# Kernel tuning notes

Measured on AMD Instinct MI355X. Metric: run time of the kernel, lower is better.

## Reference

```python
import jax, jax.numpy as jnp
import numpy as np

BN_EPS = 1e-5
NORM_EPS = 1e-12  # F.normalize eps


def setup_inputs() -> dict:
    key = jax.random.key(0)
    ks = jax.random.split(key, 4)
    B, C1, H, W = 32, 2048, 32, 32
    D1, D2, NC = 1024, 256, 1000
    x = jax.random.normal(ks[0], (B, C1, H, W), dtype=jnp.float32)
    w1 = jax.random.normal(ks[1], (D1, C1), dtype=jnp.float32) * 0.01  # init_weights normal 0.01
    gamma = jnp.ones((D1,), dtype=jnp.float32)
    beta = jnp.zeros((D1,), dtype=jnp.float32)
    w2 = jax.random.normal(ks[2], (D2, D1), dtype=jnp.float32) * 0.01
    prototypes = jax.random.normal(ks[3], (NC, D2), dtype=jnp.float32)
    return {"x": x, "w1": w1, "gamma": gamma, "beta": beta, "w2": w2, "prototypes": prototypes}


def _l2_normalize(v, axis):
    n = jnp.sqrt(jnp.sum(v * v, axis=axis, keepdims=True))
    return v / jnp.maximum(n, NORM_EPS)


def reference(x, w1, gamma, beta, w2, prototypes):
    # 1x1 conv (no bias) == channel matmul
    h = jnp.einsum('bchw,dc->bdhw', x, w1)  # [B,D1,H,W]
    # BatchNorm2d (training-mode batch stats, affine)
    mean = jnp.mean(h, axis=(0, 2, 3), keepdims=True)
    var = jnp.var(h, axis=(0, 2, 3), keepdims=True)
    h = (h - mean) * jax.lax.rsqrt(var + BN_EPS)
    h = h * gamma[None, :, None, None] + beta[None, :, None, None]
    h = jax.nn.relu(h)
    # final 1x1 conv
    f = jnp.einsum('bchw,dc->bdhw', h, w2)  # [B,D2,H,W]
    B, D, H, W = f.shape
    f = f.reshape(B, D, H * W)  # flatten(2)
    # L2-normalize over channel dim per spatial position, and prototypes per row
    f_norm = _l2_normalize(f, axis=1)           # [B,D,HW]
    p_norm = _l2_normalize(prototypes, axis=1)  # [N,D]
    # einsum('bdc,nd->bnc').sum(-1) == contract d then sum c in one fused einsum
    sim = jnp.einsum('bdc,nd->bn', f_norm, p_norm)  # [B,N]
    return sim
```

## Files before the change

kernel.cpp:

```cpp
#include <hip/hip_runtime.h>

typedef __bf16 bf16;
typedef __bf16 bf16x4 __attribute__((ext_vector_type(4)));
typedef __bf16 bf16x8 __attribute__((ext_vector_type(8)));
typedef float  f32x4  __attribute__((ext_vector_type(4)));

__device__ inline void async_copy16(void* lds, const void* g) {
  __builtin_amdgcn_global_load_lds((const __attribute__((address_space(1))) void*)g,
                                   (__attribute__((address_space(3))) void*)lds,
                                   16, 0, 0);
}

__global__ __launch_bounds__(256)
void f2bf_kernel(const float* __restrict__ in, bf16* __restrict__ out, int n4) {
  int i = blockIdx.x * 256 + threadIdx.x;
  if (i < n4) {
    float4 v = ((const float4*)in)[i];
    bf16x4 o;
    o[0] = (bf16)v.x; o[1] = (bf16)v.y; o[2] = (bf16)v.z; o[3] = (bf16)v.w;
    ((bf16x4*)out)[i] = o;
  }
}

__global__ __launch_bounds__(256)
void transpose_convert(const float* __restrict__ x, bf16* __restrict__ xb) {
  __shared__ float tile[64][65];
  const int tx = threadIdx.x & 15;
  const int ty = threadIdx.x >> 4;
  const int b   = blockIdx.z;
  const int c0  = blockIdx.y * 64;
  const int hw0 = blockIdx.x * 64;
  const float* xp = x + ((size_t)b * 2048 + c0) * 1024 + hw0;
#pragma unroll
  for (int i = 0; i < 4; ++i) {
    const int c = i * 16 + ty;
    const float4 v = *(const float4*)(xp + (size_t)c * 1024 + tx * 4);
    tile[c][tx * 4 + 0] = v.x; tile[c][tx * 4 + 1] = v.y;
    tile[c][tx * 4 + 2] = v.z; tile[c][tx * 4 + 3] = v.w;
  }
  __syncthreads();
  bf16* op = xb + ((size_t)b * 1024 + hw0) * 2048 + c0;
#pragma unroll
  for (int i = 0; i < 4; ++i) {
    const int hw = i * 16 + ty;
    bf16x4 o;
    o[0] = (bf16)tile[tx * 4 + 0][hw];
    o[1] = (bf16)tile[tx * 4 + 1][hw];
    o[2] = (bf16)tile[tx * 4 + 2][hw];
    o[3] = (bf16)tile[tx * 4 + 3][hw];
    *(bf16x4*)(op + (size_t)hw * 2048 + tx * 4) = o;
  }
}

__global__ __launch_bounds__(256, 4)
void gemm1(const bf16* __restrict__ A, const bf16* __restrict__ Bt,
           bf16* __restrict__ Cb, float* __restrict__ S1, float* __restrict__ S2) {
  __shared__ __align__(16) bf16 As[128 * 64];
  __shared__ __align__(16) bf16 Bs[128 * 64];
  const int K = 2048, N = 1024;
  const int tid  = threadIdx.x;
  const int wave = tid >> 6;
  const int lane = tid & 63;
  const int id = blockIdx.x;
  const int bm = (id & 7) * 32 + ((id >> 3) >> 3);
  const int bn = (id >> 3) & 7;
  const int wr = wave >> 1, wc = wave & 1;
  const int srow = lane >> 3;
  const int scol = (lane & 7) ^ srow;

  f32x4 acc[4][4];
#pragma unroll
  for (int r = 0; r < 4; ++r)
#pragma unroll
    for (int c = 0; c < 4; ++c) acc[r][c] = (f32x4){0.f, 0.f, 0.f, 0.f};

  const bf16* Ag = A + (size_t)(bm * 128) * K;
  const bf16* Bg = Bt + (size_t)(bn * 128) * K;

  const int mrow = lane & 15;
  const int kq = lane >> 4;
  const int sw = mrow & 7;
  const bf16* Asw = As + (wr * 64) * 64;
  const bf16* Bsw = Bs + (wc * 64) * 64;

  for (int k0 = 0; k0 < K; k0 += 64) {
#pragma unroll
    for (int j = 0; j < 4; ++j) {
      const int row = j * 32 + wave * 8;
      async_copy16((void*)(As + row * 64),
                   (const void*)(Ag + (size_t)(row + srow) * K + k0 + scol * 8));
      async_copy16((void*)(Bs + row * 64),
                   (const void*)(Bg + (size_t)(row + srow) * K + k0 + scol * 8));
    }
    __syncthreads();
#pragma unroll
    for (int kk = 0; kk < 2; ++kk) {
      bf16x8 af[4], bfr[4];
      const int lc = kk * 4 + kq;
#pragma unroll
      for (int r = 0; r < 4; ++r)
        af[r] = *(const bf16x8*)(Asw + (r * 16 + mrow) * 64 + ((lc ^ sw) * 8));
#pragma unroll
      for (int c = 0; c < 4; ++c)
        bfr[c] = *(const bf16x8*)(Bsw + (c * 16 + mrow) * 64 + ((lc ^ sw) * 8));
#pragma unroll
      for (int r = 0; r < 4; ++r)
#pragma unroll
        for (int c = 0; c < 4; ++c)
          acc[r][c] = __builtin_amdgcn_mfma_f32_16x16x32_bf16(af[r], bfr[c], acc[r][c], 0, 0, 0);
    }
    __syncthreads();
  }

  const int crow = (lane >> 4) * 4;
  const int ccol = lane & 15;
#pragma unroll
  for (int r = 0; r < 4; ++r)
#pragma unroll
    for (int c = 0; c < 4; ++c)
#pragma unroll
      for (int i = 0; i < 4; ++i) {
        const int gm = bm * 128 + wr * 64 + r * 16 + crow + i;
        const int gn = bn * 128 + wc * 64 + c * 16 + ccol;
        Cb[(size_t)gm * N + gn] = (bf16)acc[r][c][i];
      }

  float s1[4], s2[4];
#pragma unroll
  for (int c = 0; c < 4; ++c) {
    float a = 0.f, b = 0.f;
#pragma unroll
    for (int r = 0; r < 4; ++r)
#pragma unroll
      for (int i = 0; i < 4; ++i) { const float v = acc[r][c][i]; a += v; b += v * v; }
#pragma unroll
    for (int msk = 16; msk < 64; msk <<= 1) { a += __shfl_xor(a, msk, 64); b += __shfl_xor(b, msk, 64); }
    s1[c] = a; s2[c] = b;
  }
  float* S1s = (float*)As;
  float* S2s = S1s + 256;
  if ((lane & 15) == lane) {
#pragma unroll
    for (int c = 0; c < 4; ++c) {
      S1s[wr * 128 + wc * 64 + c * 16 + lane] = s1[c];
      S2s[wr * 128 + wc * 64 + c * 16 + lane] = s2[c];
    }
  }
  __syncthreads();
  if (tid < 128) {
    atomicAdd(&S1[bn * 128 + tid], S1s[tid] + S1s[128 + tid]);
    atomicAdd(&S2[bn * 128 + tid], S2s[tid] + S2s[128 + tid]);
  }
}

__global__ __launch_bounds__(256)
void bn_finalize(const float* __restrict__ S1, const float* __restrict__ S2,
                 const float* __restrict__ gamma, const float* __restrict__ beta,
                 float* __restrict__ scale, float* __restrict__ shift) {
  const int d = blockIdx.x * 256 + threadIdx.x;
  const float inv_n = 1.0f / 32768.0f;
  const float mean = S1[d] * inv_n;
  const float var  = S2[d] * inv_n - mean * mean;
  const float rstd = rsqrtf(var + 1e-5f);
  const float sc = gamma[d] * rstd;
  scale[d] = sc;
  shift[d] = beta[d] - mean * sc;
}

__global__ __launch_bounds__(512, 4)
void gemm2f(const bf16* __restrict__ A, const bf16* __restrict__ Bt,
            const float* __restrict__ scale, const float* __restrict__ shift,
            float* __restrict__ g) {
  __shared__ __align__(16) bf16 As[128 * 64];
  __shared__ __align__(16) bf16 Bs[256 * 64];
  const int K = 1024;
  const int tid  = threadIdx.x;
  const int wave = tid >> 6;
  const int lane = tid & 63;
  const int bm = blockIdx.x;
  const int wr = wave >> 2, wc = wave & 3;
  const int srow = lane >> 3;
  const int scol = (lane & 7) ^ srow;

  f32x4 acc[4][4];
#pragma unroll
  for (int r = 0; r < 4; ++r)
#pragma unroll
    for (int c = 0; c < 4; ++c) acc[r][c] = (f32x4){0.f, 0.f, 0.f, 0.f};

  const bf16* Ag = A + (size_t)(bm * 128) * K;

  const int mrow = lane & 15;
  const int kq = lane >> 4;
  const int sw = mrow & 7;
  const bf16* Asw = As + (wr * 64) * 64;
  const bf16* Bsw = Bs + (wc * 64) * 64;

  for (int k0 = 0; k0 < K; k0 += 64) {
#pragma unroll
    for (int j = 0; j < 2; ++j) {
      const int row = wave * 16 + j * 8;
      async_copy16((void*)(As + row * 64),
                   (const void*)(Ag + (size_t)(row + srow) * K + k0 + scol * 8));
    }
#pragma unroll
    for (int j = 0; j < 4; ++j) {
      const int row = wave * 32 + j * 8;
      async_copy16((void*)(Bs + row * 64),
                   (const void*)(Bt + (size_t)(row + srow) * K + k0 + scol * 8));
    }
    __syncthreads();
#pragma unroll
    for (int kk = 0; kk < 2; ++kk) {
      const int lc = kk * 4 + kq;
      const int kbase = k0 + lc * 8;
      const float4 sc0 = *(const float4*)(scale + kbase);
      const float4 sc1 = *(const float4*)(scale + kbase + 4);
      const float4 sh0 = *(const float4*)(shift + kbase);
      const float4 sh1 = *(const float4*)(shift + kbase + 4);
      const float scv[8] = {sc0.x, sc0.y, sc0.z, sc0.w, sc1.x, sc1.y, sc1.z, sc1.w};
      const float shv[8] = {sh0.x, sh0.y, sh0.z, sh0.w, sh1.x, sh1.y, sh1.z, sh1.w};
      bf16x8 af[4], bfr[4];
#pragma unroll
      for (int r = 0; r < 4; ++r) {
        bf16x8 a = *(const bf16x8*)(Asw + (r * 16 + mrow) * 64 + ((lc ^ sw) * 8));
#pragma unroll
        for (int j = 0; j < 8; ++j)
          a[j] = (bf16)fmaxf(0.f, fmaf((float)a[j], scv[j], shv[j]));
        af[r] = a;
      }
#pragma unroll
      for (int c = 0; c < 4; ++c)
        bfr[c] = *(const bf16x8*)(Bsw + (c * 16 + mrow) * 64 + ((lc ^ sw) * 8));
#pragma unroll
      for (int r = 0; r < 4; ++r)
#pragma unroll
        for (int c = 0; c < 4; ++c)
          acc[r][c] = __builtin_amdgcn_mfma_f32_16x16x32_bf16(af[r], bfr[c], acc[r][c], 0, 0, 0);
    }
    __syncthreads();
  }

  float* ss4   = (float*)As;
  float* inv_s = ss4 + 512;
  const int q = lane >> 4;
#pragma unroll
  for (int r = 0; r < 4; ++r) {
    float ssv[4];
#pragma unroll
    for (int i = 0; i < 4; ++i) {
      float s = 0.f;
#pragma unroll
      for (int c = 0; c < 4; ++c) { const float v = acc[r][c][i]; s += v * v; }
#pragma unroll
      for (int msk = 1; msk < 16; msk <<= 1) s += __shfl_xor(s, msk, 64);
      ssv[i] = s;
    }
    if ((lane & 15) == 0)
#pragma unroll
      for (int i = 0; i < 4; ++i)
        ss4[wc * 128 + wr * 64 + r * 16 + q * 4 + i] = ssv[i];
  }
  __syncthreads();
  if (tid < 128) {
    const float rs = ss4[tid] + ss4[128 + tid] + ss4[256 + tid] + ss4[384 + tid];
    inv_s[tid] = 1.0f / fmaxf(sqrtf(rs), 1e-12f);
  }
  __syncthreads();
  const int b = bm >> 3;
  const int ccol = lane & 15;
#pragma unroll
  for (int c = 0; c < 4; ++c) {
    float gl = 0.f;
#pragma unroll
    for (int r = 0; r < 4; ++r)
#pragma unroll
      for (int i = 0; i < 4; ++i)
        gl += acc[r][c][i] * inv_s[wr * 64 + r * 16 + q * 4 + i];
#pragma unroll
    for (int msk = 16; msk < 64; msk <<= 1) gl += __shfl_xor(gl, msk, 64);
    if ((lane & 48) == 0)
      atomicAdd(&g[b * 256 + wc * 64 + c * 16 + ccol], gl);
  }
}

__global__ __launch_bounds__(256)
void sim_kernel(const float* __restrict__ g, const float* __restrict__ protos,
                float* __restrict__ out) {
  const int wave = threadIdx.x >> 6, lane = threadIdx.x & 63;
  const int n = blockIdx.x * 4 + wave;
  const float4 p = *(const float4*)(protos + (size_t)n * 256 + lane * 4);
  float ss = p.x * p.x + p.y * p.y + p.z * p.z + p.w * p.w;
#pragma unroll
  for (int msk = 1; msk < 64; msk <<= 1) ss += __shfl_xor(ss, msk, 64);
  const float inv = 1.0f / fmaxf(sqrtf(ss), 1e-12f);
  const float px = p.x * inv, py = p.y * inv, pz = p.z * inv, pw = p.w * inv;
  for (int b = 0; b < 32; ++b) {
    const float4 gv = *(const float4*)(g + b * 256 + lane * 4);
    float d = px * gv.x + py * gv.y + pz * gv.z + pw * gv.w;
#pragma unroll
    for (int msk = 1; msk < 64; msk <<= 1) d += __shfl_xor(d, msk, 64);
    if (lane == 0) out[b * 1000 + n] = d;
  }
}

extern "C" void kernel_launch(void* const* d_in, const int* in_sizes, int n_in,
                              void* d_out, int out_size, void* d_ws, size_t ws_size,
                              hipStream_t stream) {
  const float* x      = (const float*)d_in[0];
  const float* w1     = (const float*)d_in[1];
  const float* gamma  = (const float*)d_in[2];
  const float* beta   = (const float*)d_in[3];
  const float* w2     = (const float*)d_in[4];
  const float* protos = (const float*)d_in[5];
  float* out = (float*)d_out;

  char* ws = (char*)d_ws;
  bf16*  xb    = (bf16*)(ws);
  bf16*  hb    = (bf16*)(ws + (size_t)134217728);
  bf16*  w1b   = (bf16*)(ws + (size_t)201326592);
  bf16*  w2b   = (bf16*)(ws + (size_t)205520896);
  float* S1    = (float*)(ws + (size_t)206045184);
  float* S2    = (float*)(ws + (size_t)206049280);
  float* g     = (float*)(ws + (size_t)206053376);
  float* scale = (float*)(ws + (size_t)206086144);
  float* shift = (float*)(ws + (size_t)206090240);

  hipMemsetAsync(S1, 0, 40960, stream);

  f2bf_kernel<<<2048, 256, 0, stream>>>(w1, w1b, 524288);
  f2bf_kernel<<<256, 256, 0, stream>>>(w2, w2b, 65536);
  transpose_convert<<<dim3(16, 32, 32), 256, 0, stream>>>(x, xb);
  gemm1<<<2048, 256, 0, stream>>>(xb, w1b, hb, S1, S2);
  bn_finalize<<<4, 256, 0, stream>>>(S1, S2, gamma, beta, scale, shift);
  gemm2f<<<256, 512, 0, stream>>>(hb, w2b, scale, shift, g);
  sim_kernel<<<250, 256, 0, stream>>>(g, protos, out);
}
```

Baseline: 612.2 us.

## Fuse x transpose and bf16 conversion into gemm1 A-tile loading

Drops the separate transpose_convert pass and has gemm1 read fp32 x directly, transposing 4x4 sub-blocks with cross-lane shuffles and writing swizzled bf16 into LDS. This removes a 256MB read plus 128MB write/read round trip of the bf16 copy of x. In exchange, gemm1 reads fp32 A (twice the bytes per tile) synchronously instead of via async LDS loads, its occupancy bound drops to 3, and the main loop carries extra shuffle work. gemm2f also stages the BN scale and shift arrays in LDS instead of reading them from global memory every k step.

```diff
diff --git a/kernel.cpp b/kernel.cpp
--- a/kernel.cpp
+++ b/kernel.cpp
@@ -9,6 +9,19 @@
   __builtin_amdgcn_global_load_lds((const __attribute__((address_space(1))) void*)g,
                                    (__attribute__((address_space(3))) void*)lds,
                                    16, 0, 0);
+}
+
+__device__ inline void xpose4(float v[4], int cg) {
+  float a = (cg & 2) ? v[0] : v[2];
+  float b = (cg & 2) ? v[1] : v[3];
+  float ra = __shfl_xor(a, 32, 64);
+  float rb = __shfl_xor(b, 32, 64);
+  if (cg & 2) { v[0] = ra; v[1] = rb; } else { v[2] = ra; v[3] = rb; }
+  float c = (cg & 1) ? v[0] : v[1];
+  float d = (cg & 1) ? v[2] : v[3];
+  float rc = __shfl_xor(c, 16, 64);
+  float rd = __shfl_xor(d, 16, 64);
+  if (cg & 1) { v[0] = rc; v[2] = rd; } else { v[1] = rc; v[3] = rd; }
 }
 
 __global__ __launch_bounds__(256)
@@ -22,38 +35,8 @@
   }
 }
 
-__global__ __launch_bounds__(256)
-void transpose_convert(const float* __restrict__ x, bf16* __restrict__ xb) {
-  __shared__ float tile[64][65];
-  const int tx = threadIdx.x & 15;
-  const int ty = threadIdx.x >> 4;
-  const int b   = blockIdx.z;
-  const int c0  = blockIdx.y * 64;
-  const int hw0 = blockIdx.x * 64;
-  const float* xp = x + ((size_t)b * 2048 + c0) * 1024 + hw0;
-#pragma unroll
-  for (int i = 0; i < 4; ++i) {
-    const int c = i * 16 + ty;
-    const float4 v = *(const float4*)(xp + (size_t)c * 1024 + tx * 4);
-    tile[c][tx * 4 + 0] = v.x; tile[c][tx * 4 + 1] = v.y;
-    tile[c][tx * 4 + 2] = v.z; tile[c][tx * 4 + 3] = v.w;
-  }
-  __syncthreads();
-  bf16* op = xb + ((size_t)b * 1024 + hw0) * 2048 + c0;
-#pragma unroll
-  for (int i = 0; i < 4; ++i) {
-    const int hw = i * 16 + ty;
-    bf16x4 o;
-    o[0] = (bf16)tile[tx * 4 + 0][hw];
-    o[1] = (bf16)tile[tx * 4 + 1][hw];
-    o[2] = (bf16)tile[tx * 4 + 2][hw];
-    o[3] = (bf16)tile[tx * 4 + 3][hw];
-    *(bf16x4*)(op + (size_t)hw * 2048 + tx * 4) = o;
-  }
-}
-
-__global__ __launch_bounds__(256, 4)
-void gemm1(const bf16* __restrict__ A, const bf16* __restrict__ Bt,
+__global__ __launch_bounds__(256, 3)
+void gemm1(const float* __restrict__ X, const bf16* __restrict__ Bt,
            bf16* __restrict__ Cb, float* __restrict__ S1, float* __restrict__ S2) {
   __shared__ __align__(16) bf16 As[128 * 64];
   __shared__ __align__(16) bf16 Bs[128 * 64];
@@ -68,13 +51,22 @@
   const int srow = lane >> 3;
   const int scol = (lane & 7) ^ srow;
 
+  const int cg  = lane >> 4;
+  const int hw4 = lane & 15;
+  const int cgq = wave >> 1;
+  const int mh  = wave & 1;
+  const int ml  = mh * 64 + hw4 * 4 + cg;
+  const int mlsw = 2 * (ml & 7);
+
   f32x4 acc[4][4];
 #pragma unroll
   for (int r = 0; r < 4; ++r)
 #pragma unroll
     for (int c = 0; c < 4; ++c) acc[r][c] = (f32x4){0.f, 0.f, 0.f, 0.f};
 
-  const bf16* Ag = A + (size_t)(bm * 128) * K;
+  const int b   = bm >> 3;
+  const int hw0 = (bm & 7) * 128;
+  const float* Xg = X + (size_t)b * 2048 * 1024 + hw0 + mh * 64 + hw4 * 4;
   const bf16* Bg = Bt + (size_t)(bn * 128) * K;
 
   const int mrow = lane & 15;
@@ -87,10 +79,26 @@
 #pragma unroll
     for (int j = 0; j < 4; ++j) {
       const int row = j * 32 + wave * 8;
-      async_copy16((void*)(As + row * 64),
-                   (const void*)(Ag + (size_t)(row + srow) * K + k0 + scol * 8));
       async_copy16((void*)(Bs + row * 64),
                    (const void*)(Bg + (size_t)(row + srow) * K + k0 + scol * 8));
+    }
+#pragma unroll
+    for (int h = 0; h < 2; ++h) {
+      float4 xa[4];
+#pragma unroll
+      for (int s = 0; s < 4; ++s) {
+        const int cq = (h * 4 + s) * 2 + cgq;
+        xa[s] = *(const float4*)(Xg + (size_t)(k0 + cq * 4 + cg) * 1024);
+      }
+#pragma unroll
+      for (int s = 0; s < 4; ++s) {
+        const int cq = (h * 4 + s) * 2 + cgq;
+        float v[4] = {xa[s].x, xa[s].y, xa[s].z, xa[s].w};
+        xpose4(v, cg);
+        bf16x4 o;
+        o[0] = (bf16)v[0]; o[1] = (bf16)v[1]; o[2] = (bf16)v[2]; o[3] = (bf16)v[3];
+        *(bf16x4*)(As + ml * 64 + (cq ^ mlsw) * 4) = o;
+      }
     }
     __syncthreads();
 #pragma unroll
@@ -128,14 +136,14 @@
   float s1[4], s2[4];
 #pragma unroll
   for (int c = 0; c < 4; ++c) {
-    float a = 0.f, b = 0.f;
+    float a = 0.f, bb = 0.f;
 #pragma unroll
     for (int r = 0; r < 4; ++r)
 #pragma unroll
-      for (int i = 0; i < 4; ++i) { const float v = acc[r][c][i]; a += v; b += v * v; }
-#pragma unroll
-    for (int msk = 16; msk < 64; msk <<= 1) { a += __shfl_xor(a, msk, 64); b += __shfl_xor(b, msk, 64); }
-    s1[c] = a; s2[c] = b;
+      for (int i = 0; i < 4; ++i) { const float v = acc[r][c][i]; a += v; bb += v * v; }
+#pragma unroll
+    for (int msk = 16; msk < 64; msk <<= 1) { a += __shfl_xor(a, msk, 64); bb += __shfl_xor(bb, msk, 64); }
+    s1[c] = a; s2[c] = bb;
   }
   float* S1s = (float*)As;
   float* S2s = S1s + 256;
@@ -173,6 +181,8 @@
             float* __restrict__ g) {
   __shared__ __align__(16) bf16 As[128 * 64];
   __shared__ __align__(16) bf16 Bs[256 * 64];
+  __shared__ __align__(16) float scs[1024];
+  __shared__ __align__(16) float shs[1024];
   const int K = 1024;
   const int tid  = threadIdx.x;
   const int wave = tid >> 6;
@@ -182,6 +192,11 @@
   const int srow = lane >> 3;
   const int scol = (lane & 7) ^ srow;
 
+  if (tid < 256) {
+    ((float4*)scs)[tid] = ((const float4*)scale)[tid];
+    ((float4*)shs)[tid] = ((const float4*)shift)[tid];
+  }
+
   f32x4 acc[4][4];
 #pragma unroll
   for (int r = 0; r < 4; ++r)
@@ -195,6 +210,7 @@
   const int sw = mrow & 7;
   const bf16* Asw = As + (wr * 64) * 64;
   const bf16* Bsw = Bs + (wc * 64) * 64;
+  __syncthreads();
 
   for (int k0 = 0; k0 < K; k0 += 64) {
 #pragma unroll
@@ -214,10 +230,10 @@
     for (int kk = 0; kk < 2; ++kk) {
       const int lc = kk * 4 + kq;
       const int kbase = k0 + lc * 8;
-      const float4 sc0 = *(const float4*)(scale + kbase);
-      const float4 sc1 = *(const float4*)(scale + kbase + 4);
-      const float4 sh0 = *(const float4*)(shift + kbase);
-      const float4 sh1 = *(const float4*)(shift + kbase + 4);
+      const float4 sc0 = *(const float4*)(scs + kbase);
+      const float4 sc1 = *(const float4*)(scs + kbase + 4);
+      const float4 sh0 = *(const float4*)(shs + kbase);
+      const float4 sh1 = *(const float4*)(shs + kbase + 4);
       const float scv[8] = {sc0.x, sc0.y, sc0.z, sc0.w, sc1.x, sc1.y, sc1.z, sc1.w};
       const float shv[8] = {sh0.x, sh0.y, sh0.z, sh0.w, sh1.x, sh1.y, sh1.z, sh1.w};
       bf16x8 af[4], bfr[4];
@@ -316,22 +332,20 @@
   float* out = (float*)d_out;
 
   char* ws = (char*)d_ws;
-  bf16*  xb    = (bf16*)(ws);
-  bf16*  hb    = (bf16*)(ws + (size_t)134217728);
-  bf16*  w1b   = (bf16*)(ws + (size_t)201326592);
-  bf16*  w2b   = (bf16*)(ws + (size_t)205520896);
-  float* S1    = (float*)(ws + (size_t)206045184);
-  float* S2    = (float*)(ws + (size_t)206049280);
-  float* g     = (float*)(ws + (size_t)206053376);
-  float* scale = (float*)(ws + (size_t)206086144);
-  float* shift = (float*)(ws + (size_t)206090240);
+  bf16*  hb    = (bf16*)(ws);
+  bf16*  w1b   = (bf16*)(ws + (size_t)67108864);
+  bf16*  w2b   = (bf16*)(ws + (size_t)71303168);
+  float* S1    = (float*)(ws + (size_t)71827456);
+  float* S2    = (float*)(ws + (size_t)71831552);
+  float* g     = (float*)(ws + (size_t)71835648);
+  float* scale = (float*)(ws + (size_t)71868416);
+  float* shift = (float*)(ws + (size_t)71872512);
 
   hipMemsetAsync(S1, 0, 40960, stream);
 
   f2bf_kernel<<<2048, 256, 0, stream>>>(w1, w1b, 524288);
   f2bf_kernel<<<256, 256, 0, stream>>>(w2, w2b, 65536);
-  transpose_convert<<<dim3(16, 32, 32), 256, 0, stream>>>(x, xb);
-  gemm1<<<2048, 256, 0, stream>>>(xb, w1b, hb, S1, S2);
+  gemm1<<<2048, 256, 0, stream>>>(x, w1b, hb, S1, S2);
   bn_finalize<<<4, 256, 0, stream>>>(S1, S2, gamma, beta, scale, shift);
   gemm2f<<<256, 512, 0, stream>>>(hb, w2b, scale, shift, g);
   sim_kernel<<<250, 256, 0, stream>>>(g, protos, out);
```

New measurement: 672.2 us. 9.8% more time.
